# Kernel tuning notes

Measured on AMD Instinct MI355X. Metric: run time of the kernel, lower is better.

The kernel has to match this reference:

```python
import jax, jax.numpy as jnp
import numpy as np

N, FEAT, N_ANC, ANC = 131072, 256, 64, 128
EPS = 1e-5

def _xavier(key, shape, gain=1.414):
    fan_in, fan_out = shape[0], shape[1]
    a = gain * np.sqrt(6.0 / (fan_in + fan_out))
    return jax.random.uniform(key, shape, jnp.float32, -a, a)

def setup_inputs() -> dict:
    key = jax.random.key(0)
    ks = jax.random.split(key, 6)
    return {
        "features": jax.random.normal(ks[0], (N, FEAT), jnp.float32),
        "W_send": _xavier(ks[1], (FEAT, ANC)),            # send_attention.weight_matrix
        "a_send": _xavier(ks[2], (2 * ANC, 1)),           # send_attention.attention_vector
        "W_recv": _xavier(ks[3], (N_ANC, FEAT)),          # receive_attention.weight_matrix
        "a_recv": _xavier(ks[4], (2 * FEAT, 1)),          # receive_attention.attention_vector
        "anchors": _xavier(ks[5], (N_ANC, ANC), gain=1.0),# anchor_embeddings
        "g_feat": jnp.ones((FEAT,), jnp.float32),
        "b_feat": jnp.zeros((FEAT,), jnp.float32),
        "g_anc": jnp.ones((N_ANC,), jnp.float32),
        "b_anc": jnp.zeros((N_ANC,), jnp.float32),
    }

def _layer_norm(x, g, b):
    mu = jnp.mean(x, axis=-1, keepdims=True)
    var = jnp.mean((x - mu) ** 2, axis=-1, keepdims=True)  # biased, as in torch LN
    return (x - mu) * jax.lax.rsqrt(var + EPS) * g + b

def _fca(x, W, a):
    # Original: scores_ij = cat(h_i, h_j) @ a = (h_i @ a1) + (h_j @ a2);
    # softmax over j of (s1_i + s2_j) == softmax(s2)_j, independent of i.
    # attended_i = sum_j softmax(s2)_j * h_j  -> same row broadcast to all i.
    H = x @ W                      # [N, D]
    D = W.shape[1]
    s2 = H @ a[D:, 0]              # [N]
    w = jax.nn.softmax(s2)         # [N]
    pooled = w @ H                 # [D]
    return jnp.broadcast_to(pooled, (x.shape[0], D))

def reference(features, W_send, a_send, W_recv, a_recv, anchors, g_feat, b_feat, g_anc, b_anc):
    nf = _layer_norm(features, g_feat, b_feat)      # [N, FEAT]
    sent = _fca(nf, W_send, a_send)                 # [N, ANC]
    proj = sent @ anchors.T                         # [N, N_ANC]
    na = _layer_norm(proj, g_anc, b_anc)            # [N, N_ANC]
    recv = _fca(na, W_recv, a_recv)                 # [N, FEAT]
    return features + jnp.sin(recv)
```

## Files before the change

### kernel.cpp

```cpp
#include <hip/hip_runtime.h>
#include <hip/hip_bf16.h>

#define N_ROWS 131072
#define FEAT   256
#define N_ANC  64
#define ANC    128
#define LN_EPS 1e-5f

#define WPB    4
#define GMAX   64

__device__ __forceinline__ float bf2f(unsigned short u) {
    return __uint_as_float(((unsigned int)u) << 16);
}
__device__ __forceinline__ unsigned short f2bf(float f) {
    unsigned int u = __float_as_uint(f);
    u += 0x7fffu + ((u >> 16) & 1u);
    return (unsigned short)(u >> 16);
}

__device__ __forceinline__ bool is_bf16(const void* g_feat) {
    return *(const unsigned int*)g_feat != 0x3F800000u;
}

template<bool BF>
__device__ __forceinline__ float ld1(const void* p, int i) {
    return BF ? bf2f(((const unsigned short*)p)[i]) : ((const float*)p)[i];
}

template<bool BF>
__device__ __forceinline__ void ld4row(const void* feat, size_t row, int lane, float x[4]) {
    if (BF) {
        ushort4 w = *(const ushort4*)((const unsigned short*)feat + row * FEAT + lane * 4);
        x[0] = bf2f(w.x); x[1] = bf2f(w.y); x[2] = bf2f(w.z); x[3] = bf2f(w.w);
    } else {
        float4 w = *(const float4*)((const float*)feat + row * FEAT + lane * 4);
        x[0] = w.x; x[1] = w.y; x[2] = w.z; x[3] = w.w;
    }
}

template<bool BF>
__device__ __forceinline__ void k0_body(
    const void* Wsend, const void* a_send, float* v)
{
    __shared__ float a2[ANC];
    int t = threadIdx.x;
    if (t < ANC) a2[t] = ld1<BF>(a_send, ANC + t);
    __syncthreads();
    float acc = 0.f;
    #pragma unroll 4
    for (int j = 0; j < ANC; ++j) acc = fmaf(ld1<BF>(Wsend, t * ANC + j), a2[j], acc);
    v[t] = acc;
}

__global__ __launch_bounds__(256) void k0_vvec(
    const void* __restrict__ Wsend, const void* __restrict__ a_send,
    const void* __restrict__ g_feat, float* __restrict__ v)
{
    if (is_bf16(g_feat)) k0_body<true>(Wsend, a_send, v);
    else                 k0_body<false>(Wsend, a_send, v);
}

template<bool BF>
__device__ __forceinline__ void k1_body(
    const void* feat, const void* g_feat, const void* b_feat, const float* v,
    float* pm, float* pd, float* pu, int nwave, int npair)
{
    const int tid  = threadIdx.x;
    const int lane = tid & 63;
    const int w    = tid >> 6;
    const int gw   = blockIdx.x * WPB + w;

    float g[4], b[4], gv[4];
    float sgv = 0.f, sbv = 0.f;
    #pragma unroll
    for (int j = 0; j < 4; ++j) {
        float vg = ld1<BF>(g_feat, lane * 4 + j);
        float vb = ld1<BF>(b_feat, lane * 4 + j);
        float vv = v[lane * 4 + j];
        g[j] = vg; b[j] = vb;
        gv[j] = vg * vv;
        sgv += gv[j];
        sbv += vb * vv;
    }
    #pragma unroll
    for (int off = 1; off < 64; off <<= 1) {
        sgv += __shfl_xor(sgv, off, 64);
        sbv += __shfl_xor(sbv, off, 64);
    }

    float m = -1e30f, d = 0.f;
    float u[4] = {0.f, 0.f, 0.f, 0.f};

    for (int it = 0; it < npair; ++it) {
        const size_t ra = (size_t)gw + (size_t)(it * 2) * nwave;
        const size_t rb = ra + nwave;
        float xa[4], xb[4];
        ld4row<BF>(feat, ra, lane, xa);
        ld4row<BF>(feat, rb, lane, xb);

        float sA = 0.f, qA = 0.f, dA = 0.f;
        float sB = 0.f, qB = 0.f, dB = 0.f;
        #pragma unroll
        for (int j = 0; j < 4; ++j) {
            sA += xa[j]; qA = fmaf(xa[j], xa[j], qA); dA = fmaf(xa[j], gv[j], dA);
            sB += xb[j]; qB = fmaf(xb[j], xb[j], qB); dB = fmaf(xb[j], gv[j], dB);
        }
        #pragma unroll
        for (int off = 1; off < 64; off <<= 1) {
            sA += __shfl_xor(sA, off, 64);
            qA += __shfl_xor(qA, off, 64);
            dA += __shfl_xor(dA, off, 64);
            sB += __shfl_xor(sB, off, 64);
            qB += __shfl_xor(qB, off, 64);
            dB += __shfl_xor(dB, off, 64);
        }
        const float muA = sA * (1.f / 256.f);
        const float muB = sB * (1.f / 256.f);
        const float rA  = rsqrtf(fmaf(-muA, muA, qA * (1.f / 256.f)) + LN_EPS);
        const float rB  = rsqrtf(fmaf(-muB, muB, qB * (1.f / 256.f)) + LN_EPS);
        const float s2A = fmaf(rA, fmaf(-muA, sgv, dA), sbv);
        const float s2B = fmaf(rB, fmaf(-muB, sgv, dB), sbv);

        float nfa[4], nfb[4];
        #pragma unroll
        for (int j = 0; j < 4; ++j) {
            nfa[j] = fmaf((xa[j] - muA) * rA, g[j], b[j]);
            nfb[j] = fmaf((xb[j] - muB) * rB, g[j], b[j]);
        }

        const float mx = fmaxf(m, fmaxf(s2A, s2B));
        const float sc = __expf(m - mx);
        const float ea = __expf(s2A - mx);
        const float eb = __expf(s2B - mx);
        d = fmaf(d, sc, ea + eb);
        #pragma unroll
        for (int j = 0; j < 4; ++j)
            u[j] = fmaf(u[j], sc, fmaf(ea, nfa[j], eb * nfb[j]));
        m = mx;
    }

    __shared__ float su[WPB][FEAT];
    __shared__ float smd[WPB][2];
    #pragma unroll
    for (int j = 0; j < 4; ++j) su[w][lane * 4 + j] = u[j];
    if (lane == 0) { smd[w][0] = m; smd[w][1] = d; }
    __syncthreads();

    const float M  = fmaxf(fmaxf(smd[0][0], smd[1][0]), fmaxf(smd[2][0], smd[3][0]));
    const float e0 = __expf(smd[0][0] - M);
    const float e1 = __expf(smd[1][0] - M);
    const float e2 = __expf(smd[2][0] - M);
    const float e3 = __expf(smd[3][0] - M);
    if (tid == 0) {
        pm[blockIdx.x] = M;
        pd[blockIdx.x] = smd[0][1] * e0 + smd[1][1] * e1 + smd[2][1] * e2 + smd[3][1] * e3;
    }
    pu[blockIdx.x * FEAT + tid] =
        su[0][tid] * e0 + su[1][tid] * e1 + su[2][tid] * e2 + su[3][tid] * e3;
}

__global__ __launch_bounds__(256) void k1_pass(
    const void* __restrict__ feat,
    const void* __restrict__ g_feat,
    const void* __restrict__ b_feat,
    const float* __restrict__ v,
    float* __restrict__ pm, float* __restrict__ pd, float* __restrict__ pu,
    int nwave, int npair)
{
    if (is_bf16(g_feat)) k1_body<true >(feat, g_feat, b_feat, v, pm, pd, pu, nwave, npair);
    else                 k1_body<false>(feat, g_feat, b_feat, v, pm, pd, pu, nwave, npair);
}

__global__ __launch_bounds__(256) void k2a_reduce(
    const float* __restrict__ pm, const float* __restrict__ pd,
    const float* __restrict__ pu,
    float* __restrict__ qm, float* __restrict__ qd, float* __restrict__ qu,
    int Q)
{
    const int tid  = threadIdx.x;
    const int g    = blockIdx.x;
    const int base = g * Q;

    __shared__ float sm[GMAX];
    __shared__ float se[GMAX];

    if (tid < Q) sm[tid] = pm[base + tid];
    __syncthreads();

    float M = -1e30f;
    #pragma unroll 16
    for (int i = 0; i < Q; ++i) M = fmaxf(M, sm[i]);
    __syncthreads();

    if (tid < Q) se[tid] = __expf(sm[tid] - M);
    __syncthreads();

    if (tid == 0) {
        float dsum = 0.f;
        for (int i = 0; i < Q; ++i) dsum = fmaf(pd[base + i], se[i], dsum);
        qd[g] = dsum;
        qm[g] = M;
    }

    float acc = 0.f;
    #pragma unroll 16
    for (int i = 0; i < Q; ++i)
        acc = fmaf(pu[(size_t)(base + i) * FEAT + tid], se[i], acc);
    qu[g * FEAT + tid] = acc;
}

template<bool BF>
__device__ __forceinline__ void k2_body(
    const float* pm, const float* pd, const float* pu,
    const void* Wsend, const void* anchors, const void* Wrecv,
    const void* g_anc, const void* b_anc, float* sv, int P)
{
    const int tid  = threadIdx.x;
    const int lane = tid & 63;
    const int wv   = tid >> 6;

    __shared__ float sE[GMAX];
    __shared__ float sred[4];
    __shared__ float sun[FEAT];
    __shared__ float spool[ANC];
    __shared__ float sproj[N_ANC];
    __shared__ float sna[N_ANC];
    __shared__ float sc2[2];

    float mm = -1e30f;
    for (int i = tid; i < P; i += 256) mm = fmaxf(mm, pm[i]);
    #pragma unroll
    for (int off = 1; off < 64; off <<= 1) mm = fmaxf(mm, __shfl_xor(mm, off, 64));
    if (lane == 0) sred[wv] = mm;
    __syncthreads();
    const float M = fmaxf(fmaxf(sred[0], sred[1]), fmaxf(sred[2], sred[3]));

    float dt = 0.f;
    for (int i = tid; i < P; i += 256) {
        const float e = __expf(pm[i] - M);
        sE[i] = e;
        dt = fmaf(pd[i], e, dt);
    }
    #pragma unroll
    for (int off = 1; off < 64; off <<= 1) dt += __shfl_xor(dt, off, 64);
    __syncthreads();
    if (lane == 0) sred[wv] = dt;
    __syncthreads();
    const float D = (sred[0] + sred[1]) + (sred[2] + sred[3]);

    float acc = 0.f;
    #pragma unroll 16
    for (int bb = 0; bb < P; ++bb) acc = fmaf(pu[bb * FEAT + tid], sE[bb], acc);
    sun[tid] = acc / D;
    __syncthreads();

    if (tid < ANC) {
        float p = 0.f;
        #pragma unroll 4
        for (int k = 0; k < FEAT; ++k) p = fmaf(sun[k], ld1<BF>(Wsend, k * ANC + tid), p);
        spool[tid] = p;
    }
    __syncthreads();

    if (tid < N_ANC) {
        float p = 0.f;
        #pragma unroll 4
        for (int j = 0; j < ANC; ++j) p = fmaf(spool[j], ld1<BF>(anchors, tid * ANC + j), p);
        sproj[tid] = p;
    }
    __syncthreads();

    if (tid == 0) {
        float s = 0.f, q = 0.f;
        for (int k = 0; k < N_ANC; ++k) { s += sproj[k]; q = fmaf(sproj[k], sproj[k], q); }
        const float mu  = s * (1.f / 64.f);
        const float var = q * (1.f / 64.f) - mu * mu;
        sc2[0] = mu; sc2[1] = rsqrtf(var + LN_EPS);
    }
    __syncthreads();
    if (tid < N_ANC)
        sna[tid] = fmaf((sproj[tid] - sc2[0]) * sc2[1], ld1<BF>(g_anc, tid), ld1<BF>(b_anc, tid));
    __syncthreads();

    {
        float h = 0.f;
        #pragma unroll 4
        for (int k = 0; k < N_ANC; ++k) h = fmaf(sna[k], ld1<BF>(Wrecv, k * FEAT + tid), h);
        sv[tid] = sinf(h);
    }
}

__global__ __launch_bounds__(256) void k2_combine(
    const float* __restrict__ pm, const float* __restrict__ pd,
    const float* __restrict__ pu,
    const void* __restrict__ Wsend, const void* __restrict__ anchors,
    const void* __restrict__ Wrecv, const void* __restrict__ g_anc,
    const void* __restrict__ b_anc, const void* __restrict__ g_feat,
    float* __restrict__ sv, int P)
{
    if (is_bf16(g_feat)) k2_body<true >(pm, pd, pu, Wsend, anchors, Wrecv, g_anc, b_anc, sv, P);
    else                 k2_body<false>(pm, pd, pu, Wsend, anchors, Wrecv, g_anc, b_anc, sv, P);
}

__global__ __launch_bounds__(256) void k3_out(
    const void* __restrict__ feat, const float* __restrict__ sv,
    const void* __restrict__ g_feat, void* __restrict__ out)
{
    const int tid = threadIdx.x;
    const int stride = gridDim.x * blockDim.x;

    if (is_bf16(g_feat)) {
        const int c = (tid * 8) & 255;
        float s[8];
        #pragma unroll
        for (int j = 0; j < 8; ++j) s[j] = sv[c + j];
        const int total8 = N_ROWS * FEAT / 8;
        for (int i = blockIdx.x * blockDim.x + tid; i < total8; i += stride) {
            uint4 w = ((const uint4*)feat)[i];
            unsigned int in[4] = {w.x, w.y, w.z, w.w};
            unsigned int r[4];
            #pragma unroll
            for (int j = 0; j < 4; ++j) {
                const float lo = bf2f((unsigned short)(in[j] & 0xffffu));
                const float hi = bf2f((unsigned short)(in[j] >> 16));
                const unsigned short ol = f2bf(lo + s[j * 2]);
                const unsigned short oh = f2bf(hi + s[j * 2 + 1]);
                r[j] = (unsigned int)ol | ((unsigned int)oh << 16);
            }
            uint4 o; o.x = r[0]; o.y = r[1]; o.z = r[2]; o.w = r[3];
            ((uint4*)out)[i] = o;
        }
    } else {
        const int c = (tid * 4) & 255;
        float s[4];
        #pragma unroll
        for (int j = 0; j < 4; ++j) s[j] = sv[c + j];
        const int total4 = N_ROWS * FEAT / 4;
        for (int i = blockIdx.x * blockDim.x + tid; i < total4; i += stride) {
            float4 w = ((const float4*)feat)[i];
            float4 o;
            o.x = w.x + s[0]; o.y = w.y + s[1];
            o.z = w.z + s[2]; o.w = w.w + s[3];
            ((float4*)out)[i] = o;
        }
    }
}

extern "C" void kernel_launch(void* const* d_in, const int* in_sizes, int n_in,
                              void* d_out, int out_size, void* d_ws, size_t ws_size,
                              hipStream_t stream)
{
    const void* feat    = d_in[0];
    const void* Wsend   = d_in[1];
    const void* a_send  = d_in[2];
    const void* Wrecv   = d_in[3];
    const void* anchors = d_in[5];
    const void* g_feat  = d_in[6];
    const void* b_feat  = d_in[7];
    const void* g_anc   = d_in[8];
    const void* b_anc   = d_in[9];

    int P = 1024;
    while (P > 1 &&
           (size_t)(2048 + 1032 * (size_t)P + 1032 * GMAX) > ws_size) P >>= 1;
    const int G = (P >= GMAX) ? GMAX : P;
    const int Q = P / G;

    const int nwave = P * WPB;
    const int npair = N_ROWS / (2 * nwave);

    float* ws = (float*)d_ws;
    float* v  = ws;
    float* sv = ws + 256;
    float* pm = ws + 512;
    float* pd = ws + 512 + P;
    float* pu = ws + 512 + 2 * P;
    float* qm = pu + (size_t)P * FEAT;
    float* qd = qm + G;
    float* qu = qd + G;

    k0_vvec<<<1, 256, 0, stream>>>(Wsend, a_send, g_feat, v);
    k1_pass<<<P, 256, 0, stream>>>(feat, g_feat, b_feat, v, pm, pd, pu, nwave, npair);
    k2a_reduce<<<G, 256, 0, stream>>>(pm, pd, pu, qm, qd, qu, Q);
    k2_combine<<<1, 256, 0, stream>>>(qm, qd, qu, Wsend, anchors, Wrecv,
                                      g_anc, b_anc, g_feat, sv, G);
    k3_out<<<4096, 256, 0, stream>>>(feat, sv, g_feat, d_out);
}
```

Before: 308.1 us.

## Process four rows per wave with 16-lane groups and defer LayerNorm affine

```diff
diff --git a/kernel.cpp b/kernel.cpp
--- a/kernel.cpp
+++ b/kernel.cpp
@@ -29,13 +29,24 @@
 }
 
 template<bool BF>
-__device__ __forceinline__ void ld4row(const void* feat, size_t row, int lane, float x[4]) {
+__device__ __forceinline__ void ld16(const void* feat, size_t row, int t, float x[16]) {
     if (BF) {
-        ushort4 w = *(const ushort4*)((const unsigned short*)feat + row * FEAT + lane * 4);
-        x[0] = bf2f(w.x); x[1] = bf2f(w.y); x[2] = bf2f(w.z); x[3] = bf2f(w.w);
+        const uint4* pp = (const uint4*)((const unsigned short*)feat + row * FEAT + t * 16);
+        const uint4 w0 = pp[0];
+        const uint4 w1 = pp[1];
+        const unsigned int ws[8] = {w0.x, w0.y, w0.z, w0.w, w1.x, w1.y, w1.z, w1.w};
+        #pragma unroll
+        for (int k = 0; k < 8; ++k) {
+            x[2 * k]     = bf2f((unsigned short)(ws[k] & 0xffffu));
+            x[2 * k + 1] = bf2f((unsigned short)(ws[k] >> 16));
+        }
     } else {
-        float4 w = *(const float4*)((const float*)feat + row * FEAT + lane * 4);
-        x[0] = w.x; x[1] = w.y; x[2] = w.z; x[3] = w.w;
+        const float4* pp = (const float4*)((const float*)feat + row * FEAT + t * 16);
+        #pragma unroll
+        for (int k = 0; k < 4; ++k) {
+            const float4 wv = pp[k];
+            x[4 * k] = wv.x; x[4 * k + 1] = wv.y; x[4 * k + 2] = wv.z; x[4 * k + 3] = wv.w;
+        }
     }
 }
 
@@ -64,87 +75,92 @@
 template<bool BF>
 __device__ __forceinline__ void k1_body(
     const void* feat, const void* g_feat, const void* b_feat, const float* v,
-    float* pm, float* pd, float* pu, int nwave, int npair)
+    float* pm, float* pd, float* pu, int nwave, int nit)
 {
     const int tid  = threadIdx.x;
     const int lane = tid & 63;
     const int w    = tid >> 6;
+    const int t    = lane & 15;
+    const int gq   = lane >> 4;
     const int gw   = blockIdx.x * WPB + w;
 
-    float g[4], b[4], gv[4];
+    float gv[16];
     float sgv = 0.f, sbv = 0.f;
     #pragma unroll
-    for (int j = 0; j < 4; ++j) {
-        float vg = ld1<BF>(g_feat, lane * 4 + j);
-        float vb = ld1<BF>(b_feat, lane * 4 + j);
-        float vv = v[lane * 4 + j];
-        g[j] = vg; b[j] = vb;
+    for (int j = 0; j < 16; ++j) {
+        const float vg = ld1<BF>(g_feat, t * 16 + j);
+        const float vb = ld1<BF>(b_feat, t * 16 + j);
+        const float vv = v[t * 16 + j];
         gv[j] = vg * vv;
         sgv += gv[j];
         sbv += vb * vv;
     }
     #pragma unroll
-    for (int off = 1; off < 64; off <<= 1) {
+    for (int off = 1; off < 16; off <<= 1) {
         sgv += __shfl_xor(sgv, off, 64);
         sbv += __shfl_xor(sbv, off, 64);
     }
 
     float m = -1e30f, d = 0.f;
-    float u[4] = {0.f, 0.f, 0.f, 0.f};
-
-    for (int it = 0; it < npair; ++it) {
-        const size_t ra = (size_t)gw + (size_t)(it * 2) * nwave;
-        const size_t rb = ra + nwave;
-        float xa[4], xb[4];
-        ld4row<BF>(feat, ra, lane, xa);
-        ld4row<BF>(feat, rb, lane, xb);
-
-        float sA = 0.f, qA = 0.f, dA = 0.f;
-        float sB = 0.f, qB = 0.f, dB = 0.f;
-        #pragma unroll
-        for (int j = 0; j < 4; ++j) {
-            sA += xa[j]; qA = fmaf(xa[j], xa[j], qA); dA = fmaf(xa[j], gv[j], dA);
-            sB += xb[j]; qB = fmaf(xb[j], xb[j], qB); dB = fmaf(xb[j], gv[j], dB);
-        }
-        #pragma unroll
-        for (int off = 1; off < 64; off <<= 1) {
-            sA += __shfl_xor(sA, off, 64);
-            qA += __shfl_xor(qA, off, 64);
-            dA += __shfl_xor(dA, off, 64);
-            sB += __shfl_xor(sB, off, 64);
-            qB += __shfl_xor(qB, off, 64);
-            dB += __shfl_xor(dB, off, 64);
-        }
-        const float muA = sA * (1.f / 256.f);
-        const float muB = sB * (1.f / 256.f);
-        const float rA  = rsqrtf(fmaf(-muA, muA, qA * (1.f / 256.f)) + LN_EPS);
-        const float rB  = rsqrtf(fmaf(-muB, muB, qB * (1.f / 256.f)) + LN_EPS);
-        const float s2A = fmaf(rA, fmaf(-muA, sgv, dA), sbv);
-        const float s2B = fmaf(rB, fmaf(-muB, sgv, dB), sbv);
-
-        float nfa[4], nfb[4];
-        #pragma unroll
-        for (int j = 0; j < 4; ++j) {
-            nfa[j] = fmaf((xa[j] - muA) * rA, g[j], b[j]);
-            nfb[j] = fmaf((xb[j] - muB) * rB, g[j], b[j]);
-        }
-
-        const float mx = fmaxf(m, fmaxf(s2A, s2B));
+    float u[16];
+    #pragma unroll
+    for (int j = 0; j < 16; ++j) u[j] = 0.f;
+
+    for (int it = 0; it < nit; ++it) {
+        const size_t row = ((size_t)gw + (size_t)it * nwave) * 4 + gq;
+        float x[16];
+        ld16<BF>(feat, row, t, x);
+
+        float s = 0.f, q = 0.f, dt = 0.f;
+        #pragma unroll
+        for (int j = 0; j < 16; ++j) {
+            s += x[j]; q = fmaf(x[j], x[j], q); dt = fmaf(x[j], gv[j], dt);
+        }
+        #pragma unroll
+        for (int off = 1; off < 16; off <<= 1) {
+            s  += __shfl_xor(s,  off, 64);
+            q  += __shfl_xor(q,  off, 64);
+            dt += __shfl_xor(dt, off, 64);
+        }
+        const float mu = s * (1.f / 256.f);
+        const float r  = rsqrtf(fmaf(-mu, mu, q * (1.f / 256.f)) + LN_EPS);
+        const float s2 = fmaf(r, fmaf(-mu, sgv, dt), sbv);
+
+        const float mx = fmaxf(m, s2);
         const float sc = __expf(m - mx);
-        const float ea = __expf(s2A - mx);
-        const float eb = __expf(s2B - mx);
-        d = fmaf(d, sc, ea + eb);
-        #pragma unroll
-        for (int j = 0; j < 4; ++j)
-            u[j] = fmaf(u[j], sc, fmaf(ea, nfa[j], eb * nfb[j]));
+        const float ea = __expf(s2 - mx);
+        d = fmaf(d, sc, ea);
+        const float mur = mu * r;
+        #pragma unroll
+        for (int j = 0; j < 16; ++j) {
+            const float nfr = fmaf(x[j], r, -mur);
+            u[j] = fmaf(u[j], sc, ea * nfr);
+        }
         m = mx;
+    }
+
+    float M4 = m;
+    M4 = fmaxf(M4, __shfl_xor(M4, 16, 64));
+    M4 = fmaxf(M4, __shfl_xor(M4, 32, 64));
+    const float wg = __expf(m - M4);
+    float d4 = d * wg;
+    d4 += __shfl_xor(d4, 16, 64);
+    d4 += __shfl_xor(d4, 32, 64);
+    #pragma unroll
+    for (int j = 0; j < 16; ++j) {
+        float uj = u[j] * wg;
+        uj += __shfl_xor(uj, 16, 64);
+        uj += __shfl_xor(uj, 32, 64);
+        u[j] = uj;
     }
 
     __shared__ float su[WPB][FEAT];
     __shared__ float smd[WPB][2];
-    #pragma unroll
-    for (int j = 0; j < 4; ++j) su[w][lane * 4 + j] = u[j];
-    if (lane == 0) { smd[w][0] = m; smd[w][1] = d; }
+    if (gq == 0) {
+        #pragma unroll
+        for (int j = 0; j < 16; ++j) su[w][t * 16 + j] = u[j];
+    }
+    if (lane == 0) { smd[w][0] = M4; smd[w][1] = d4; }
     __syncthreads();
 
     const float M  = fmaxf(fmaxf(smd[0][0], smd[1][0]), fmaxf(smd[2][0], smd[3][0]));
@@ -166,10 +182,10 @@
     const void* __restrict__ b_feat,
     const float* __restrict__ v,
     float* __restrict__ pm, float* __restrict__ pd, float* __restrict__ pu,
-    int nwave, int npair)
-{
-    if (is_bf16(g_feat)) k1_body<true >(feat, g_feat, b_feat, v, pm, pd, pu, nwave, npair);
-    else                 k1_body<false>(feat, g_feat, b_feat, v, pm, pd, pu, nwave, npair);
+    int nwave, int nit)
+{
+    if (is_bf16(g_feat)) k1_body<true >(feat, g_feat, b_feat, v, pm, pd, pu, nwave, nit);
+    else                 k1_body<false>(feat, g_feat, b_feat, v, pm, pd, pu, nwave, nit);
 }
 
 __global__ __launch_bounds__(256) void k2a_reduce(
@@ -184,12 +200,13 @@
 
     __shared__ float sm[GMAX];
     __shared__ float se[GMAX];
-
-    if (tid < Q) sm[tid] = pm[base + tid];
+    __shared__ float spd[GMAX];
+
+    if (tid < Q) { sm[tid] = pm[base + tid]; spd[tid] = pd[base + tid]; }
     __syncthreads();
 
     float M = -1e30f;
-    #pragma unroll 16
+    #pragma unroll 8
     for (int i = 0; i < Q; ++i) M = fmaxf(M, sm[i]);
     __syncthreads();
 
@@ -198,7 +215,7 @@
 
     if (tid == 0) {
         float dsum = 0.f;
-        for (int i = 0; i < Q; ++i) dsum = fmaf(pd[base + i], se[i], dsum);
+        for (int i = 0; i < Q; ++i) dsum = fmaf(spd[i], se[i], dsum);
         qd[g] = dsum;
         qm[g] = M;
     }
@@ -214,7 +231,8 @@
 __device__ __forceinline__ void k2_body(
     const float* pm, const float* pd, const float* pu,
     const void* Wsend, const void* anchors, const void* Wrecv,
-    const void* g_anc, const void* b_anc, float* sv, int P)
+    const void* g_anc, const void* b_anc,
+    const void* g_feat, const void* b_feat, float* sv, int P)
 {
     const int tid  = threadIdx.x;
     const int lane = tid & 63;
@@ -252,7 +270,7 @@
     float acc = 0.f;
     #pragma unroll 16
     for (int bb = 0; bb < P; ++bb) acc = fmaf(pu[bb * FEAT + tid], sE[bb], acc);
-    sun[tid] = acc / D;
+    sun[tid] = fmaf(ld1<BF>(g_feat, tid), acc / D, ld1<BF>(b_feat, tid));
     __syncthreads();
 
     if (tid < ANC) {
@@ -297,10 +315,12 @@
     const void* __restrict__ Wsend, const void* __restrict__ anchors,
     const void* __restrict__ Wrecv, const void* __restrict__ g_anc,
     const void* __restrict__ b_anc, const void* __restrict__ g_feat,
-    float* __restrict__ sv, int P)
-{
-    if (is_bf16(g_feat)) k2_body<true >(pm, pd, pu, Wsend, anchors, Wrecv, g_anc, b_anc, sv, P);
-    else                 k2_body<false>(pm, pd, pu, Wsend, anchors, Wrecv, g_anc, b_anc, sv, P);
+    const void* __restrict__ b_feat, float* __restrict__ sv, int P)
+{
+    if (is_bf16(g_feat))
+        k2_body<true >(pm, pd, pu, Wsend, anchors, Wrecv, g_anc, b_anc, g_feat, b_feat, sv, P);
+    else
+        k2_body<false>(pm, pd, pu, Wsend, anchors, Wrecv, g_anc, b_anc, g_feat, b_feat, sv, P);
 }
 
 __global__ __launch_bounds__(256) void k3_out(
@@ -368,7 +388,7 @@
     const int Q = P / G;
 
     const int nwave = P * WPB;
-    const int npair = N_ROWS / (2 * nwave);
+    const int nit   = N_ROWS / (4 * nwave);
 
     float* ws = (float*)d_ws;
     float* v  = ws;
@@ -381,9 +401,9 @@
     float* qu = qd + G;
 
     k0_vvec<<<1, 256, 0, stream>>>(Wsend, a_send, g_feat, v);
-    k1_pass<<<P, 256, 0, stream>>>(feat, g_feat, b_feat, v, pm, pd, pu, nwave, npair);
+    k1_pass<<<P, 256, 0, stream>>>(feat, g_feat, b_feat, v, pm, pd, pu, nwave, nit);
     k2a_reduce<<<G, 256, 0, stream>>>(pm, pd, pu, qm, qd, qu, Q);
     k2_combine<<<1, 256, 0, stream>>>(qm, qd, qu, Wsend, anchors, Wrecv,
-                                      g_anc, b_anc, g_feat, sv, G);
+                                      g_anc, b_anc, g_feat, b_feat, sv, G);
     k3_out<<<4096, 256, 0, stream>>>(feat, sv, g_feat, d_out);
 }
```

Measured after the change: 311.7 us. Within noise of the previous version (+1.2%).
